# Kernel tuning notes

Measured on AMD Instinct MI355X. Metric: run time of the kernel, lower is better.

Reference implementation:

```python
import jax, jax.numpy as jnp
import numpy as np

ALPHA = 0.2  # LeakyReLU negative slope
NEG_INF = -9e15


def setup_inputs() -> dict:
    key = jax.random.key(0)
    k1, k2, k3, k4 = jax.random.split(key, 4)
    B, N, Fin, Fout = 4, 4096, 256, 128
    h = jax.random.normal(k1, (B, N, Fin), dtype=jnp.float32)
    adj = jax.random.randint(k2, (B, N, N), 0, 2, dtype=jnp.int32)  # {0,1} adjacency
    # xavier_uniform with gain 1.414
    limW = 1.414 * np.sqrt(6.0 / (Fin + Fout))
    W = jax.random.uniform(k3, (Fin, Fout), jnp.float32, -limW, limW)
    lima = 1.414 * np.sqrt(6.0 / (2 * Fout + 1))
    a = jax.random.uniform(k4, (2 * Fout, 1), jnp.float32, -lima, lima)
    return {"h": h, "adj": adj, "W": W, "a": a}


def reference(h, adj, W, a):
    # Wh: [B, N, Fout]
    Wh = jnp.einsum('bni,io->bno', h, W)
    Fout = W.shape[1]
    # Decompose a^T [Wh_i || Wh_j] = a1.Wh_i + a2.Wh_j (identical math, avoids
    # materializing the [B,N,N,2F] concat tensor the torch code builds).
    a1, a2 = a[:Fout, 0], a[Fout:, 0]
    s1 = jnp.einsum('bno,o->bn', Wh, a1)  # [B, N]
    s2 = jnp.einsum('bno,o->bn', Wh, a2)  # [B, N]
    e = jax.nn.leaky_relu(s1[:, :, None] + s2[:, None, :], negative_slope=ALPHA)  # [B,N,N]
    attention = jnp.where(adj > 0, e, jnp.asarray(NEG_INF, e.dtype))
    attention = jax.nn.softmax(attention, axis=2)
    # dropout is inactive in eval mode (training=False)
    # Faithful to the torch code: the FIRST h_prime is overwritten; the output is
    # einsum('bjk,bji->bki', attention, Wh) -> sums over the softmax (row) axis j.
    h_prime = jnp.einsum('bjk,bji->bki', attention, Wh)  # [B, N, Fout]
    return jax.nn.elu(h_prime)  # concat=True
```

## Files before the change

### kernel.cpp

```cpp
#include <hip/hip_runtime.h>
#include <hip/hip_bf16.h>

#define ALPHA 0.2f
#define L2E 1.4426950408889634f

constexpr int Nn = 4096;
constexpr int FIN = 256;
constexpr int FOUT = 128;
constexpr int JC = 8;
constexpr int JQ = 512;
constexpr int NCH = 16;
constexpr long long SLAB = 2097152;

typedef __attribute__((ext_vector_type(8))) short short8;
typedef __attribute__((ext_vector_type(8))) unsigned short ushort8;
typedef __attribute__((ext_vector_type(4))) float f32x4;
typedef __attribute__((ext_vector_type(16))) float f32x16;
typedef __attribute__((ext_vector_type(4))) int int4v;

__device__ __forceinline__ unsigned short f2bf(float x) {
  unsigned int u = __float_as_uint(x);
  unsigned int r = (u + 0x7fffu + ((u >> 16) & 1u)) >> 16;
  return (unsigned short)r;
}

__device__ __forceinline__ float bf2f(unsigned short v) {
  return __uint_as_float(((unsigned)v) << 16);
}

__device__ __forceinline__ void gload16(const void* g, void* l) {
  auto lp = (__attribute__((address_space(3))) void*)l;
  auto gp = (const __attribute__((address_space(1))) void*)g;
  __builtin_amdgcn_global_load_lds(gp, lp, 16, 0, 0);
}

__global__ __launch_bounds__(256) void k0_prep(
    const float* __restrict__ W, unsigned short* __restrict__ WT) {
  __shared__ float lw[32][132];
  int t = threadIdx.x;
  int kc0 = blockIdx.x * 32;
#pragma unroll
  for (int m = 0; m < 4; ++m) {
    int idx = t * 16 + m * 4;
    f32x4 v = *(const f32x4*)(W + kc0 * 128 + idx);
    int k = idx >> 7, i0 = idx & 127;
    *(f32x4*)&lw[k][i0] = v;
  }
  __syncthreads();
  int i = t >> 1, half = t & 1;
  unsigned short pk[16];
#pragma unroll
  for (int kk = 0; kk < 16; ++kk) pk[kk] = f2bf(lw[half * 16 + kk][i]);
  ushort8* dst = (ushort8*)(WT + i * 256 + kc0 + half * 16);
  dst[0] = *(ushort8*)&pk[0];
  dst[1] = *(ushort8*)&pk[8];
}

__global__ __launch_bounds__(256) void k1b_wh(
    const float* __restrict__ h, const unsigned short* __restrict__ WT,
    const float* __restrict__ a, unsigned short* __restrict__ whT,
    float* __restrict__ s1L, float* __restrict__ s2L) {
  __shared__ __align__(16) char smem[36864];
  int t = threadIdx.x;
  int w = t >> 6, l = t & 63, g = l >> 4, r = l & 15;
  int r0 = blockIdx.x * 16;
  int b = r0 >> 12, nbase = r0 & 4095;

  f32x4 acc[2];
  acc[0] = (f32x4){0.f, 0.f, 0.f, 0.f};
  acc[1] = (f32x4){0.f, 0.f, 0.f, 0.f};

  for (int kc = 0; kc < 2; ++kc) {
    __syncthreads();
    {
      int row = t >> 4, sec = t & 15;
      const f32x4* src =
          (const f32x4*)(h + (long long)(r0 + row) * 256 + kc * 128 + sec * 8);
      f32x4 v0 = src[0], v1 = src[1];
      unsigned int pk[4];
      pk[0] = ((unsigned)f2bf(v0.y) << 16) | f2bf(v0.x);
      pk[1] = ((unsigned)f2bf(v0.w) << 16) | f2bf(v0.z);
      pk[2] = ((unsigned)f2bf(v1.y) << 16) | f2bf(v1.x);
      pk[3] = ((unsigned)f2bf(v1.w) << 16) | f2bf(v1.z);
      *(ushort8*)(smem + row * 256 + ((sec ^ (row & 7)) << 4)) = *(ushort8*)pk;
    }
    {
      int i = t >> 1, pt = t & 1;
      const ushort8* src = (const ushort8*)(WT + i * 256 + kc * 128 + pt * 64);
#pragma unroll
      for (int m = 0; m < 8; ++m) {
        ushort8 v = src[m];
        int slot = pt * 8 + m;
        *(ushort8*)(smem + 4096 + i * 256 + ((slot ^ (i & 7)) << 4)) = v;
      }
    }
    __syncthreads();
#pragma unroll
    for (int kk = 0; kk < 4; ++kk) {
      short8 af =
          *(const short8*)(smem + r * 256 + (((kk * 4 + g) ^ (r & 7)) << 4));
#pragma unroll
      for (int s = 0; s < 2; ++s) {
        int i = w * 32 + s * 16 + r;
        short8 bf = *(const short8*)(smem + 4096 + i * 256 +
                                     (((kk * 4 + g) ^ (i & 7)) << 4));
        acc[s] =
            __builtin_amdgcn_mfma_f32_16x16x32_bf16(af, bf, acc[s], 0, 0, 0);
      }
    }
  }

  __syncthreads();
  unsigned short* tb = (unsigned short*)smem;
#pragma unroll
  for (int s = 0; s < 2; ++s)
#pragma unroll
    for (int q = 0; q < 4; ++q)
      tb[(w * 32 + s * 16 + r) * 24 + g * 4 + q] = f2bf(acc[s][q]);
  __syncthreads();

  {
    int i = t >> 1, half = t & 1;
    ushort8 v = *(const ushort8*)(tb + i * 24 + half * 8);
    *(ushort8*)(whT + (((long long)(b * 128 + i)) << 12) + nbase + half * 8) =
        v;
  }
  {
    int n = t >> 4, seg = t & 15;
    f32x4 a10 = *(const f32x4*)(a + seg * 8);
    f32x4 a11 = *(const f32x4*)(a + seg * 8 + 4);
    f32x4 a20 = *(const f32x4*)(a + 128 + seg * 8);
    f32x4 a21 = *(const f32x4*)(a + 128 + seg * 8 + 4);
    float v1 = 0.f, v2 = 0.f;
#pragma unroll
    for (int m = 0; m < 8; ++m) {
      float wh = bf2f(tb[(seg * 8 + m) * 24 + n]);
      float c1 = (m < 4) ? a10[m] : a11[m - 4];
      float c2 = (m < 4) ? a20[m] : a21[m - 4];
      v1 += wh * c1;
      v2 += wh * c2;
    }
#pragma unroll
    for (int off = 8; off; off >>= 1) {
      v1 += __shfl_xor(v1, off);
      v2 += __shfl_xor(v2, off);
    }
    if (seg == 0) {
      s1L[r0 + n] = v1 * L2E;
      s2L[r0 + n] = v2 * L2E;
    }
  }
}

__global__ __launch_bounds__(256) void k2_stats(
    const int* __restrict__ adj, const float* __restrict__ s1L,
    const float* __restrict__ s2L, float2* __restrict__ st2,
    unsigned long long* __restrict__ mask64) {
  __shared__ unsigned int mwords[128];
  __shared__ float wsum[4];
  int row = blockIdx.x;
  int b = row >> 12;
  int t = threadIdx.x;
  float s1j = s1L[row];
  const int4v* arow = (const int4v*)(adj + (long long)row * Nn);
  const f32x4* s2v = (const f32x4*)(s2L + (b << 12));

  float sum = 0.f;
#pragma unroll
  for (int q = 0; q < 4; ++q) {
    int4v av = __builtin_nontemporal_load(arow + q * 256 + t);
    f32x4 sv = s2v[q * 256 + t];
    unsigned nib = 0;
#pragma unroll
    for (int c = 0; c < 4; ++c) {
      float u = s1j + sv[c];
      float vL = fmaxf(u, ALPHA * u);
      float e = exp2f(vL);
      sum += (av[c] > 0) ? e : 0.f;
      nib |= ((unsigned)(av[c] > 0)) << c;
    }
    unsigned n1 = nib | (__shfl_xor(nib, 1) << 4);
    unsigned n2 = n1 | (__shfl_xor(n1, 2) << 8);
    unsigned n4 = n2 | (__shfl_xor(n2, 4) << 16);
    if ((t & 7) == 0) mwords[q * 32 + (t >> 3)] = n4;
  }
#pragma unroll
  for (int off = 32; off; off >>= 1) sum += __shfl_xor(sum, off);
  if ((t & 63) == 0) wsum[t >> 6] = sum;
  __syncthreads();
  if (t < 64) {
    unsigned long long mv = *(unsigned long long*)&mwords[t * 2];
    mask64[((long long)row << 6) + t] = mv;
  }
  if (t == 0) {
    float S = wsum[0] + wsum[1] + wsum[2] + wsum[3];
    float negc = (S > 0.f) ? -log2f(S) : -1.0e30f;
    st2[row] = make_float2(s1j + negc, ALPHA * s1j + negc);
  }
}

__global__ __launch_bounds__(512, 4) void k3_pv(
    const unsigned short* __restrict__ whT, const float2* __restrict__ st2,
    const unsigned long long* __restrict__ mask64,
    const float* __restrict__ s2L, unsigned short* __restrict__ pbuf) {
  __shared__ __align__(16) char smem[36864];
  char* mbase = smem + 16384;
  float2* stl = (float2*)(smem + 32768);

  int t = threadIdx.x;
  int orig = blockIdx.x;
  int swz = (orig & 7) * 64 + (orig >> 3);
  int kt = swz & 15, jc = (swz >> 4) & 7, b = swz >> 7;
  int w = t >> 6, l = t & 63, hl = l >> 5, ln = l & 31;
  int jq0 = jc * JQ;
  long long brow = (long long)(b << 12);
  int k0 = kt << 8;
  float z1 = s2L[brow + k0 + w * 32 + ln];
  float z2 = ALPHA * z1;

  if (t < 256) gload16(st2 + brow + jq0 + t * 2, (char*)stl + t * 16);
  {
    const char* msrc = (const char*)(mask64 + ((brow + jq0 + t) << 6) + kt * 4);
    gload16(msrc, mbase + t * 16);
    gload16(msrc + 16, mbase + 8192 + t * 16);
  }
  const unsigned short* whTb = whT + ((long long)b << 19);
  int gj = t >> 7, gi = t & 127;
  const unsigned short* wsrc = whTb + (long long)gi * 4096 + jq0 + gj * 8;
  gload16(wsrc, smem + t * 16);
  __syncthreads();

  char* mwv = mbase + (w >> 2) * 8192 + (w & 3) * 4;

  f32x16 acc[4];
#pragma unroll
  for (int q = 0; q < 4; ++q)
#pragma unroll
    for (int r = 0; r < 16; ++r) acc[q][r] = 0.f;

  for (int ch = 0; ch < NCH; ++ch) {
    int cur = ch & 1;
    if (ch + 1 < NCH)
      gload16(wsrc + (ch + 1) * 32, smem + (cur ^ 1) * 8192 + t * 16);
    char* wb = smem + cur * 8192;
    int jb = ch * 32 + hl * 8;
#pragma unroll
    for (int s = 0; s < 2; ++s) {
      short8 af;
#pragma unroll
      for (int e = 0; e < 8; ++e) {
        int ja = jb + s * 16 + e;
        float2 sc = stl[ja];
        unsigned int mv = *(unsigned int*)(mwv + ja * 16);
        float e1 = sc.x + z1;
        float e2 = sc.y + z2;
        float p = exp2f(fmaxf(e1, e2));
        p = ((mv >> ln) & 1u) ? p : 0.f;
        __hip_bfloat16 hb = __float2bfloat16(p);
        af[e] = *(short*)&hb;
      }
      int gbase = (2 * s + hl) * 2048;
#pragma unroll
      for (int q = 0; q < 4; ++q) {
        short8 bv = *(const short8*)(wb + gbase + ((q * 32 + ln) << 4));
        acc[q] =
            __builtin_amdgcn_mfma_f32_32x32x16_bf16(af, bv, acc[q], 0, 0, 0);
      }
    }
    __syncthreads();
  }

  unsigned short* pb = pbuf + (long long)jc * SLAB + ((brow + k0) << 7);
#pragma unroll
  for (int q = 0; q < 4; ++q) {
#pragma unroll
    for (int r = 0; r < 16; ++r) {
      int kl = (r & 3) + ((r >> 2) << 3) + (hl << 2) + (w << 5);
      __builtin_nontemporal_store(f2bf(acc[q][r]),
                                  pb + kl * 128 + q * 32 + ln);
    }
  }
}

__global__ __launch_bounds__(256) void k4_reduce(
    const unsigned short* __restrict__ pbuf, float* __restrict__ out) {
  int base = (blockIdx.x * 256 + threadIdx.x) * 8;
  float s[8] = {0.f, 0.f, 0.f, 0.f, 0.f, 0.f, 0.f, 0.f};
#pragma unroll
  for (int sl = 0; sl < JC; ++sl) {
    ushort8 v = __builtin_nontemporal_load(
        (const ushort8*)(pbuf + (long long)sl * SLAB + base));
#pragma unroll
    for (int e = 0; e < 8; ++e)
      s[e] += __uint_as_float(((unsigned)(unsigned short)v[e]) << 16);
  }
  f32x4 o0, o1;
#pragma unroll
  for (int e = 0; e < 8; ++e) {
    float x = s[e];
    float y = x > 0.f ? x : expm1f(x);
    if (e < 4) o0[e] = y; else o1[e - 4] = y;
  }
  *(f32x4*)(out + base) = o0;
  *(f32x4*)(out + base + 4) = o1;
}

extern "C" void kernel_launch(void* const* d_in, const int* in_sizes, int n_in,
                              void* d_out, int out_size, void* d_ws,
                              size_t ws_size, hipStream_t stream) {
  const float* h = (const float*)d_in[0];
  const int* adj = (const int*)d_in[1];
  const float* W = (const float*)d_in[2];
  const float* a = (const float*)d_in[3];
  float* out = (float*)d_out;

  char* ws = (char*)d_ws;
  unsigned short* WT = (unsigned short*)ws;
  unsigned short* whT = (unsigned short*)(ws + (1 << 20));
  float* s1L = (float*)(ws + (5 << 20));
  float* s2L = s1L + 16384;
  float2* st2 = (float2*)(ws + (5 << 20) + (128 << 10));
  unsigned long long* mask64 =
      (unsigned long long*)(ws + (6 << 20));
  unsigned short* pbuf = (unsigned short*)(ws + (16 << 20));

  hipLaunchKernelGGL(k0_prep, dim3(8), dim3(256), 0, stream, W, WT);
  hipLaunchKernelGGL(k1b_wh, dim3(1024), dim3(256), 0, stream, h, WT, a, whT,
                     s1L, s2L);
  hipLaunchKernelGGL(k2_stats, dim3(16384), dim3(256), 0, stream, adj, s1L,
                     s2L, st2, mask64);
  hipLaunchKernelGGL(k3_pv, dim3(512), dim3(512), 0, stream, whT, st2, mask64,
                     s2L, pbuf);
  hipLaunchKernelGGL(k4_reduce, dim3(1024), dim3(256), 0, stream, pbuf, out);
}
```

Before: 122.3 us.

## Halve j-chunk count in PV kernel with in-block split-j reduction

The PV kernel now covers 1024 j per block instead of 512, with 128 k rows per block instead of 256. The j dimension is split across two wave groups whose partial accumulators are summed through shared memory before a single store. This halves the number of partial slabs that the reduce kernel must read and sum. It also pads the transpose staging stride in the first kernel to avoid LDS bank conflicts, swizzles block order in the reduce kernel, and replaces the bit-test select with an arithmetic mask. The trade-off is extra LDS traffic and a barrier for the in-block reduction, plus a longer per-block serial loop.

```diff
diff --git a/kernel.cpp b/kernel.cpp
--- a/kernel.cpp
+++ b/kernel.cpp
@@ -7,9 +7,9 @@
 constexpr int Nn = 4096;
 constexpr int FIN = 256;
 constexpr int FOUT = 128;
-constexpr int JC = 8;
-constexpr int JQ = 512;
-constexpr int NCH = 16;
+constexpr int JC = 4;
+constexpr int JQ = 1024;
+constexpr int NCH = 32;
 constexpr long long SLAB = 2097152;
 
 typedef __attribute__((ext_vector_type(8))) short short8;
@@ -116,12 +116,12 @@
   for (int s = 0; s < 2; ++s)
 #pragma unroll
     for (int q = 0; q < 4; ++q)
-      tb[(w * 32 + s * 16 + r) * 24 + g * 4 + q] = f2bf(acc[s][q]);
+      tb[(w * 32 + s * 16 + r) * 25 + g * 4 + q] = f2bf(acc[s][q]);
   __syncthreads();
 
   {
     int i = t >> 1, half = t & 1;
-    ushort8 v = *(const ushort8*)(tb + i * 24 + half * 8);
+    ushort8 v = *(const ushort8*)(tb + i * 25 + half * 8);
     *(ushort8*)(whT + (((long long)(b * 128 + i)) << 12) + nbase + half * 8) =
         v;
   }
@@ -134,7 +134,7 @@
     float v1 = 0.f, v2 = 0.f;
 #pragma unroll
     for (int m = 0; m < 8; ++m) {
-      float wh = bf2f(tb[(seg * 8 + m) * 24 + n]);
+      float wh = bf2f(tb[(seg * 8 + m) * 25 + n]);
       float c1 = (m < 4) ? a10[m] : a11[m - 4];
       float c2 = (m < 4) ? a20[m] : a21[m - 4];
       v1 += wh * c1;
@@ -203,34 +203,40 @@
     const unsigned short* __restrict__ whT, const float2* __restrict__ st2,
     const unsigned long long* __restrict__ mask64,
     const float* __restrict__ s2L, unsigned short* __restrict__ pbuf) {
-  __shared__ __align__(16) char smem[36864];
+  __shared__ __align__(16) char smem[40960];
   char* mbase = smem + 16384;
   float2* stl = (float2*)(smem + 32768);
 
   int t = threadIdx.x;
   int orig = blockIdx.x;
-  int swz = (orig & 7) * 64 + (orig >> 3);
-  int kt = swz & 15, jc = (swz >> 4) & 7, b = swz >> 7;
+  int x = orig & 7, mm = orig >> 3;
+  int b = x >> 1;
+  int kt = ((x & 1) << 4) | (mm & 15);
+  int jc = mm >> 4;
   int w = t >> 6, l = t & 63, hl = l >> 5, ln = l & 31;
+  int ks = w & 3, jh = w >> 2;
   int jq0 = jc * JQ;
   long long brow = (long long)(b << 12);
-  int k0 = kt << 8;
-  float z1 = s2L[brow + k0 + w * 32 + ln];
+  int k0 = kt << 7;
+  float z1 = s2L[brow + k0 + ks * 32 + ln];
   float z2 = ALPHA * z1;
-
-  if (t < 256) gload16(st2 + brow + jq0 + t * 2, (char*)stl + t * 16);
+  int sh31 = 31 - ln;
+
+  gload16(st2 + brow + jq0 + t * 2, (char*)stl + t * 16);
   {
-    const char* msrc = (const char*)(mask64 + ((brow + jq0 + t) << 6) + kt * 4);
-    gload16(msrc, mbase + t * 16);
-    gload16(msrc + 16, mbase + 8192 + t * 16);
+    const char* m0 =
+        (const char*)(mask64 + ((brow + jq0 + t) << 6)) + kt * 16;
+    const char* m1 =
+        (const char*)(mask64 + ((brow + jq0 + 512 + t) << 6)) + kt * 16;
+    gload16(m0, mbase + t * 16);
+    gload16(m1, mbase + 8192 + t * 16);
   }
   const unsigned short* whTb = whT + ((long long)b << 19);
-  int gj = t >> 7, gi = t & 127;
-  const unsigned short* wsrc = whTb + (long long)gi * 4096 + jq0 + gj * 8;
-  gload16(wsrc, smem + t * 16);
-  __syncthreads();
-
-  char* mwv = mbase + (w >> 2) * 8192 + (w & 3) * 4;
+  int joct0 = t >> 7, gi = t & 127;
+  const unsigned short* wsrc0 =
+      whTb + (long long)gi * 4096 + jq0 + joct0 * 8;
+  gload16(wsrc0, smem + t * 16);
+  __syncthreads();
 
   f32x16 acc[4];
 #pragma unroll
@@ -241,55 +247,64 @@
   for (int ch = 0; ch < NCH; ++ch) {
     int cur = ch & 1;
     if (ch + 1 < NCH)
-      gload16(wsrc + (ch + 1) * 32, smem + (cur ^ 1) * 8192 + t * 16);
+      gload16(wsrc0 + (ch + 1) * 32, smem + (cur ^ 1) * 8192 + t * 16);
     char* wb = smem + cur * 8192;
-    int jb = ch * 32 + hl * 8;
-#pragma unroll
-    for (int s = 0; s < 2; ++s) {
-      short8 af;
-#pragma unroll
-      for (int e = 0; e < 8; ++e) {
-        int ja = jb + s * 16 + e;
-        float2 sc = stl[ja];
-        unsigned int mv = *(unsigned int*)(mwv + ja * 16);
-        float e1 = sc.x + z1;
-        float e2 = sc.y + z2;
-        float p = exp2f(fmaxf(e1, e2));
-        p = ((mv >> ln) & 1u) ? p : 0.f;
-        __hip_bfloat16 hb = __float2bfloat16(p);
-        af[e] = *(short*)&hb;
+    int jb = ch * 32 + jh * 16 + hl * 8;
+    short8 af;
+#pragma unroll
+    for (int e = 0; e < 8; ++e) {
+      int ja = jb + e;
+      float2 sc = stl[ja];
+      unsigned int mv = *(unsigned int*)(mbase + ja * 16 + ks * 4);
+      float e1 = sc.x + z1;
+      float e2 = sc.y + z2;
+      float p = exp2f(fmaxf(e1, e2));
+      int msk = ((int)(mv << sh31)) >> 31;
+      unsigned pu = __float_as_uint(p) & (unsigned)msk;
+      af[e] = (short)f2bf(__uint_as_float(pu));
+    }
+    int gb = (jh * 2 + hl) * 2048;
+#pragma unroll
+    for (int q = 0; q < 4; ++q) {
+      short8 bv = *(const short8*)(wb + gb + ((q * 32 + ln) << 4));
+      acc[q] = __builtin_amdgcn_mfma_f32_32x32x16_bf16(af, bv, acc[q], 0, 0, 0);
+    }
+    __syncthreads();
+  }
+
+  unsigned short* zone = (unsigned short*)smem;
+  if (jh == 1) {
+#pragma unroll
+    for (int q = 0; q < 4; ++q)
+#pragma unroll
+      for (int r = 0; r < 16; ++r) {
+        int kl = (r & 3) + ((r >> 2) << 3) + (hl << 2);
+        zone[ks * 4096 + q * 1024 + kl * 32 + ln] = f2bf(acc[q][r]);
       }
-      int gbase = (2 * s + hl) * 2048;
-#pragma unroll
-      for (int q = 0; q < 4; ++q) {
-        short8 bv = *(const short8*)(wb + gbase + ((q * 32 + ln) << 4));
-        acc[q] =
-            __builtin_amdgcn_mfma_f32_32x32x16_bf16(af, bv, acc[q], 0, 0, 0);
+  }
+  __syncthreads();
+  if (jh == 0) {
+    unsigned short* pb = pbuf + (long long)jc * SLAB + ((brow + k0) << 7);
+#pragma unroll
+    for (int q = 0; q < 4; ++q)
+#pragma unroll
+      for (int r = 0; r < 16; ++r) {
+        int kl = (r & 3) + ((r >> 2) << 3) + (hl << 2);
+        float v = acc[q][r] + bf2f(zone[ks * 4096 + q * 1024 + kl * 32 + ln]);
+        pb[(ks * 32 + kl) * 128 + q * 32 + ln] = f2bf(v);
       }
-    }
-    __syncthreads();
-  }
-
-  unsigned short* pb = pbuf + (long long)jc * SLAB + ((brow + k0) << 7);
-#pragma unroll
-  for (int q = 0; q < 4; ++q) {
-#pragma unroll
-    for (int r = 0; r < 16; ++r) {
-      int kl = (r & 3) + ((r >> 2) << 3) + (hl << 2) + (w << 5);
-      __builtin_nontemporal_store(f2bf(acc[q][r]),
-                                  pb + kl * 128 + q * 32 + ln);
-    }
   }
 }
 
 __global__ __launch_bounds__(256) void k4_reduce(
     const unsigned short* __restrict__ pbuf, float* __restrict__ out) {
-  int base = (blockIdx.x * 256 + threadIdx.x) * 8;
+  int orig = blockIdx.x;
+  int n = (orig & 7) * 128 + (orig >> 3);
+  int base = (n * 256 + threadIdx.x) * 8;
   float s[8] = {0.f, 0.f, 0.f, 0.f, 0.f, 0.f, 0.f, 0.f};
 #pragma unroll
   for (int sl = 0; sl < JC; ++sl) {
-    ushort8 v = __builtin_nontemporal_load(
-        (const ushort8*)(pbuf + (long long)sl * SLAB + base));
+    ushort8 v = *(const ushort8*)(pbuf + (long long)sl * SLAB + base);
 #pragma unroll
     for (int e = 0; e < 8; ++e)
       s[e] += __uint_as_float(((unsigned)(unsigned short)v[e]) << 16);
@@ -297,8 +312,8 @@
   f32x4 o0, o1;
 #pragma unroll
   for (int e = 0; e < 8; ++e) {
-    float x = s[e];
-    float y = x > 0.f ? x : expm1f(x);
+    float xv = s[e];
+    float y = xv > 0.f ? xv : expm1f(xv);
     if (e < 4) o0[e] = y; else o1[e - 4] = y;
   }
   *(f32x4*)(out + base) = o0;
```

Result: no change. 123.6 us (+1.0%).
